# Optimization experiments

Measured on AMD Instinct MI355X. Metric: run time of the kernel, lower is better.

Reference implementation:

```python
import jax, jax.numpy as jnp
import numpy as np

D_MODEL, D_STATE, D_CONV, EXPAND = 1024, 16, 4, 2
D_INNER = EXPAND * D_MODEL  # 2048
DT_RANK = (D_MODEL + 15) // 16  # 64
BATCH, SEQ = 2, 2048


def setup_inputs() -> dict:
    key = jax.random.key(0)
    ks = jax.random.split(key, 8)
    s = 0.02
    A = jnp.tile(jnp.arange(1, D_STATE + 1, dtype=jnp.float32), (D_INNER, 1))
    return {
        "x": jax.random.normal(ks[0], (BATCH, SEQ, D_MODEL), jnp.float32),
        "in_proj_w": jax.random.normal(ks[1], (D_MODEL, 2 * D_INNER), jnp.float32) * s,
        "conv_w": jax.random.normal(ks[2], (D_INNER, 1, D_CONV), jnp.float32) * s,
        "conv_b": jnp.zeros((D_INNER,), jnp.float32),
        "x_proj_w": jax.random.normal(ks[3], (D_INNER, DT_RANK + 2 * D_STATE), jnp.float32) * s,
        "dt_proj_w": jax.random.normal(ks[4], (DT_RANK, D_INNER), jnp.float32) * s,
        "dt_proj_b": jnp.zeros((D_INNER,), jnp.float32),
        "A_log": jnp.log(A),
        "D": jnp.ones((D_INNER,), jnp.float32),
        "out_proj_w": jax.random.normal(ks[5], (D_INNER, D_MODEL), jnp.float32) * s,
    }


def _mamba(x, in_proj_w, conv_w, conv_b, x_proj_w, dt_proj_w, dt_proj_b, A_log, D, out_proj_w):
    d_inner, d_state = A_log.shape
    dt_rank = dt_proj_w.shape[0]
    seq_len = x.shape[1]

    xr = x @ in_proj_w                       # (B, L, 2*ED)
    xb, res = jnp.split(xr, 2, axis=-1)      # each (B, L, ED)

    # causal depthwise conv1d (torch pads both sides then truncates to seq_len
    # == left-pad-only causal conv)
    xc = jnp.swapaxes(xb, 1, 2)              # (B, ED, L)
    xc = jax.lax.conv_general_dilated(
        xc, conv_w, window_strides=(1,),
        padding=[(conv_w.shape[-1] - 1, 0)],
        dimension_numbers=("NCH", "OIH", "NCH"),
        feature_group_count=d_inner)
    xc = xc + conv_b[None, :, None]
    u = jax.nn.silu(jnp.swapaxes(xc, 1, 2))  # (B, L, ED)

    dbc = u @ x_proj_w                       # (B, L, dt_rank + 2*N)
    dt, Bc, Cc = jnp.split(dbc, [dt_rank, dt_rank + d_state], axis=-1)
    dt = jax.nn.softplus(dt @ dt_proj_w + dt_proj_b)  # (B, L, ED)
    A = -jnp.exp(A_log)                      # (ED, N)

    def step(h, xs):
        dt_i, B_i, C_i, u_i = xs             # (B,ED), (B,N), (B,N), (B,ED)
        dA = jnp.exp(dt_i[:, :, None] * A)   # (B, ED, N)
        h = h * dA + (dt_i * u_i)[:, :, None] * B_i[:, None, :]
        y = jnp.einsum("bdn,bn->bd", h, C_i) + D * u_i
        return h, y

    h0 = jnp.zeros((x.shape[0], d_inner, d_state), x.dtype)
    xs = (jnp.swapaxes(dt, 0, 1), jnp.swapaxes(Bc, 0, 1),
          jnp.swapaxes(Cc, 0, 1), jnp.swapaxes(u, 0, 1))
    _, ys = jax.lax.scan(step, h0, xs)       # ys: (L, B, ED)
    y_ssm = jnp.swapaxes(ys, 0, 1)           # (B, L, ED)

    y = y_ssm * jax.nn.silu(res)
    return y @ out_proj_w                    # (B, L, d_model)


def reference(x, in_proj_w, conv_w, conv_b, x_proj_w, dt_proj_w, dt_proj_b, A_log, D, out_proj_w):
    return _mamba(x, in_proj_w, conv_w, conv_b, x_proj_w, dt_proj_w, dt_proj_b, A_log, D, out_proj_w)
```

## Files before the change

### kernel.cpp

```cpp
#include <hip/hip_runtime.h>
#include <cstddef>
#include <cstdint>

#define BATCH 2
#define SEQ   2048
#define DM    1024
#define ED    2048
#define NS    16
#define DR    64
#define NROWS (BATCH*SEQ)

#define NCHUNK 64
#define CLEN   32
#define CSTATES (BATCH*ED*NS)

#define OFF_XBH   ((size_t)0)
#define OFF_RESH  ((size_t)4194304)
#define OFF_PS    ((size_t)8388608)
#define OFF_DT    ((size_t)16777216)
#define OFF_DBC   ((size_t)25165824)
#define OFF_PART  ((size_t)25559040)

typedef _Float16 half8 __attribute__((ext_vector_type(8)));
typedef _Float16 half4 __attribute__((ext_vector_type(4)));
typedef float    floatx4 __attribute__((ext_vector_type(4)));

__device__ __forceinline__ float silu_f(float x) { return x / (1.f + __expf(-x)); }

__device__ __forceinline__ void gload_lds16(const _Float16* g, _Float16* l) {
  __builtin_amdgcn_global_load_lds(
      (const __attribute__((address_space(1))) void*)g,
      (__attribute__((address_space(3))) void*)l, 16, 0, 0);
}

template<int BN, int WGM, int WGN, int EPI, int KSPLIT, int BK>
__global__ __launch_bounds__(256)
void hgemm(const _Float16* __restrict__ A, int lda,
           const _Float16* __restrict__ Bt, int ldb,
           const float* __restrict__ bias,
           float* __restrict__ C, _Float16* __restrict__ Ch,
           _Float16* __restrict__ Ch2,
           size_t cslice, int N, int K) {
  constexpr int BM = 128;
  constexpr int FM = BM / 16 / WGM;
  constexpr int FN = BN / 16 / WGN;
  constexpr int CPR = BK / 8;
  __shared__ _Float16 sA[BM * BK];
  __shared__ _Float16 sB[BN * BK];
  const int tid = threadIdx.x;
  const int ln  = tid & 63;
  const int wid = tid >> 6;
  const int wm  = wid % WGM;
  const int wn  = wid / WGM;
  const int m0  = blockIdx.y * BM;
  const int n0  = blockIdx.x * BN;
  const int l15 = ln & 15;
  const int q   = ln >> 4;

  const int kLen = K / KSPLIT;
  const int kbeg = blockIdx.z * kLen;
  if (KSPLIT > 1) C += (size_t)blockIdx.z * cslice;

  floatx4 acc[FM][FN];
  #pragma unroll
  for (int i = 0; i < FM; ++i)
    #pragma unroll
    for (int j = 0; j < FN; ++j)
      acc[i][j] = floatx4{0.f, 0.f, 0.f, 0.f};

  for (int k0 = kbeg; k0 < kbeg + kLen; k0 += BK) {
    __syncthreads();
    #pragma unroll
    for (int s = 0; s < (BM * CPR) / 256; ++s) {
      const int i = s * 256 + tid;
      const int m = i / CPR;
      const int cg = (i & (CPR - 1)) ^ ((m >> 1) & (CPR - 1));
      gload_lds16(A + (size_t)(m0 + m) * lda + k0 + cg * 8, sA + i * 8);
    }
    #pragma unroll
    for (int s = 0; s < (BN * CPR) / 256; ++s) {
      const int i = s * 256 + tid;
      const int n = i / CPR;
      const int cg = (i & (CPR - 1)) ^ ((n >> 1) & (CPR - 1));
      gload_lds16(Bt + (size_t)(n0 + n) * ldb + k0 + cg * 8, sB + i * 8);
    }
    __syncthreads();

    #pragma unroll
    for (int h = 0; h < BK / 32; ++h) {
      half8 af[FM], bf[FN];
      #pragma unroll
      for (int fm = 0; fm < FM; ++fm) {
        const int mr = wm * FM * 16 + fm * 16 + l15;
        const int cl = (h * 4 + q) ^ ((mr >> 1) & (CPR - 1));
        af[fm] = *(const half8*)(sA + mr * BK + cl * 8);
      }
      #pragma unroll
      for (int fn = 0; fn < FN; ++fn) {
        const int nr = wn * FN * 16 + fn * 16 + l15;
        const int cl = (h * 4 + q) ^ ((nr >> 1) & (CPR - 1));
        bf[fn] = *(const half8*)(sB + nr * BK + cl * 8);
      }
      #pragma unroll
      for (int fm = 0; fm < FM; ++fm)
        #pragma unroll
        for (int fn = 0; fn < FN; ++fn)
          acc[fm][fn] = __builtin_amdgcn_mfma_f32_16x16x32_f16(
              af[fm], bf[fn], acc[fm][fn], 0, 0, 0);
    }
  }

  #pragma unroll
  for (int fm = 0; fm < FM; ++fm) {
    #pragma unroll
    for (int fn = 0; fn < FN; ++fn) {
      const int col = n0 + wn * FN * 16 + fn * 16 + l15;
      #pragma unroll
      for (int r = 0; r < 4; ++r) {
        const int row = m0 + wm * FM * 16 + fm * 16 + q * 4 + r;
        float v = acc[fm][fn][r];
        if (EPI == 2) {
          if (col < ED) Ch[(size_t)row * ED + col] = (_Float16)v;
          else          Ch2[(size_t)row * ED + (col - ED)] = (_Float16)silu_f(v);
        } else if (EPI == 3) {
          v += bias[col];
          v = fmaxf(v, 0.f) + log1pf(__expf(-fabsf(v)));
          Ch[(size_t)row * N + col] = (_Float16)v;
        } else {
          C[(size_t)row * N + col] = v;
        }
      }
    }
  }
}

__device__ __forceinline__ void transpose_tile(const float* __restrict__ src,
                                               _Float16* __restrict__ dst,
                                               int R, int C, int bx, int by,
                                               int tid) {
  __shared__ float t[32][33];
  const int tx = tid & 31, ty = tid >> 5;
  const int c0 = bx * 32, r0 = by * 32;
  #pragma unroll
  for (int s = 0; s < 4; ++s)
    t[ty + s * 8][tx] = src[(size_t)(r0 + ty + s * 8) * C + c0 + tx];
  __syncthreads();
  #pragma unroll
  for (int s = 0; s < 4; ++s)
    dst[(size_t)(c0 + ty + s * 8) * R + r0 + tx] = (_Float16)t[tx][ty + s * 8];
}

#define PREP_BLOCKS 10560
__global__ __launch_bounds__(256)
void prep_kernel(const float* __restrict__ x, _Float16* __restrict__ x_h,
                 const float* __restrict__ Win, _Float16* __restrict__ Wint,
                 const float* __restrict__ Wout, _Float16* __restrict__ Woutt,
                 const float* __restrict__ Wx, _Float16* __restrict__ Wxt,
                 const float* __restrict__ Wdt, _Float16* __restrict__ Wdtt) {
  const int bid = blockIdx.x, tid = threadIdx.x;
  if (bid < 4096) {
    const int i = bid * 1024 + tid * 4;
    const float4 v = *(const float4*)(x + i);
    half4 o;
    o[0] = (_Float16)v.x; o[1] = (_Float16)v.y;
    o[2] = (_Float16)v.z; o[3] = (_Float16)v.w;
    *(half4*)(x_h + i) = o;
  } else if (bid < 8192) {
    const int t = bid - 4096;
    transpose_tile(Win, Wint, DM, 2 * ED, t & 127, t >> 7, tid);
  } else if (bid < 10240) {
    const int t = bid - 8192;
    transpose_tile(Wout, Woutt, ED, DM, t & 31, t >> 5, tid);
  } else if (bid < 10432) {
    const int t = bid - 10240;
    transpose_tile(Wx, Wxt, ED, 96, t % 3, t / 3, tid);
  } else {
    const int t = bid - 10432;
    transpose_tile(Wdt, Wdtt, DR, ED, t & 63, t >> 6, tid);
  }
}

__global__ __launch_bounds__(256)
void conv_silu_kernel(const _Float16* __restrict__ xbh, const float* __restrict__ w,
                      const float* __restrict__ cb, _Float16* __restrict__ u_h) {
  const int idx = blockIdx.x * 256 + threadIdx.x;
  const int d = idx & (ED - 1);
  const int t = (idx >> 11) & (SEQ - 1);
  const float4 wv = ((const float4*)w)[d];
  const _Float16* base = xbh + (size_t)(idx >> 11) * ED + d;
  float acc = cb[d];
  acc = fmaf(wv.w, (float)base[0], acc);
  if (t >= 1) acc = fmaf(wv.z, (float)base[-ED], acc);
  if (t >= 2) acc = fmaf(wv.y, (float)base[-2 * ED], acc);
  if (t >= 3) acc = fmaf(wv.x, (float)base[-3 * ED], acc);
  u_h[idx] = (_Float16)silu_f(acc);
}

__global__ __launch_bounds__(256)
void xproj_reduce(const float* __restrict__ part, float* __restrict__ dbc,
                  _Float16* __restrict__ dbc64h) {
  const int idx = blockIdx.x * 256 + threadIdx.x;
  float s = 0.f;
  #pragma unroll
  for (int r = 0; r < 8; ++r) s += part[(size_t)r * NROWS * 96 + idx];
  dbc[idx] = s;
  const int col = idx % 96;
  if (col < DR) dbc64h[(idx / 96) * DR + col] = (_Float16)s;
}

__device__ __forceinline__ void conv_init_h(const _Float16* xbp, int tg0,
                                            float& x1, float& x2, float& x3) {
  x1 = (tg0 >= 1) ? (float)xbp[-(int)ED] : 0.f;
  x2 = (tg0 >= 2) ? (float)xbp[-2 * (int)ED] : 0.f;
  x3 = (tg0 >= 3) ? (float)xbp[-3 * (int)ED] : 0.f;
}

__global__ __launch_bounds__(256)
void scan2_summary(const _Float16* __restrict__ dth, const _Float16* __restrict__ xbh,
                   const float* __restrict__ convw, const float* __restrict__ convb,
                   const float* __restrict__ dbc, const float* __restrict__ A_log,
                   float* __restrict__ Pbuf, float* __restrict__ Sbuf) {
  const int d = blockIdx.x * 256 + threadIdx.x;
  const int b = blockIdx.y;
  const int g = blockIdx.z;

  float Adn[16];
  {
    const float4* al = (const float4*)(A_log + (size_t)d * NS);
    #pragma unroll
    for (int i = 0; i < 4; ++i) {
      const float4 v = al[i];
      Adn[i * 4 + 0] = -__expf(v.x); Adn[i * 4 + 1] = -__expf(v.y);
      Adn[i * 4 + 2] = -__expf(v.z); Adn[i * 4 + 3] = -__expf(v.w);
    }
  }
  const float4 wv = ((const float4*)convw)[d];
  const float cbd = convb[d];

  float P[16], S[16];
  #pragma unroll
  for (int n = 0; n < 16; ++n) { P[n] = 1.f; S[n] = 0.f; }

  const int tg0 = g * CLEN;
  const size_t row0 = (size_t)b * SEQ + tg0;
  const _Float16* dtp = dth + row0 * ED + d;
  const _Float16* xbp = xbh + row0 * ED + d;
  float x1, x2, x3;
  conv_init_h(xbp, tg0, x1, x2, x3);

  for (int t = 0; t < CLEN; ++t) {
    const float xt  = (float)xbp[(size_t)t * ED];
    const float dti = (float)dtp[(size_t)t * ED];
    float cv = cbd;
    cv = fmaf(wv.w, xt, cv);
    cv = fmaf(wv.z, x1, cv);
    cv = fmaf(wv.y, x2, cv);
    cv = fmaf(wv.x, x3, cv);
    const float ui = silu_f(cv);
    x3 = x2; x2 = x1; x1 = xt;

    const float4* bc = (const float4*)(dbc + (row0 + t) * 96 + DR);
    float Bv[16];
    #pragma unroll
    for (int i = 0; i < 4; ++i) {
      const float4 v = bc[i];
      Bv[i * 4 + 0] = v.x; Bv[i * 4 + 1] = v.y;
      Bv[i * 4 + 2] = v.z; Bv[i * 4 + 3] = v.w;
    }
    const float dtu = dti * ui;
    #pragma unroll
    for (int n = 0; n < 16; ++n) {
      const float a = __expf(dti * Adn[n]);
      S[n] = fmaf(S[n], a, dtu * Bv[n]);
      P[n] *= a;
    }
  }
  const size_t c0 = (size_t)g * CSTATES + ((size_t)(b * ED + d)) * NS;
  #pragma unroll
  for (int i = 0; i < 4; ++i) {
    *(float4*)(Pbuf + c0 + i * 4) = float4{P[i*4], P[i*4+1], P[i*4+2], P[i*4+3]};
    *(float4*)(Sbuf + c0 + i * 4) = float4{S[i*4], S[i*4+1], S[i*4+2], S[i*4+3]};
  }
}

__global__ __launch_bounds__(256)
void scan2_compose(float* __restrict__ Pbuf, const float* __restrict__ Sbuf) {
  const unsigned c = blockIdx.x * 256 + threadIdx.x;
  float h = 0.f;
  for (int g = 0; g < NCHUNK; ++g) {
    const size_t idx = (size_t)g * CSTATES + c;
    const float p = Pbuf[idx], s = Sbuf[idx];
    Pbuf[idx] = h;
    h = fmaf(p, h, s);
  }
}

__global__ __launch_bounds__(256)
void scan2_apply(const _Float16* __restrict__ dth, const _Float16* __restrict__ xbh,
                 const float* __restrict__ convw, const float* __restrict__ convb,
                 const float* __restrict__ dbc, const float* __restrict__ A_log,
                 const float* __restrict__ Dp, const float* __restrict__ Pbuf,
                 _Float16* __restrict__ resh) {
  const int d = blockIdx.x * 256 + threadIdx.x;
  const int b = blockIdx.y;
  const int g = blockIdx.z;

  float Adn[16];
  {
    const float4* al = (const float4*)(A_log + (size_t)d * NS);
    #pragma unroll
    for (int i = 0; i < 4; ++i) {
      const float4 v = al[i];
      Adn[i * 4 + 0] = -__expf(v.x); Adn[i * 4 + 1] = -__expf(v.y);
      Adn[i * 4 + 2] = -__expf(v.z); Adn[i * 4 + 3] = -__expf(v.w);
    }
  }
  const float4 wv = ((const float4*)convw)[d];
  const float cbd = convb[d];
  const float Dd = Dp[d];

  float h[16];
  const size_t c0 = (size_t)g * CSTATES + ((size_t)(b * ED + d)) * NS;
  #pragma unroll
  for (int i = 0; i < 4; ++i) {
    const float4 v = *(const float4*)(Pbuf + c0 + i * 4);
    h[i * 4 + 0] = v.x; h[i * 4 + 1] = v.y;
    h[i * 4 + 2] = v.z; h[i * 4 + 3] = v.w;
  }

  const int tg0 = g * CLEN;
  const size_t row0 = (size_t)b * SEQ + tg0;
  const _Float16* dtp = dth + row0 * ED + d;
  const _Float16* xbp = xbh + row0 * ED + d;
  _Float16* rp = resh + row0 * ED + d;
  float x1, x2, x3;
  conv_init_h(xbp, tg0, x1, x2, x3);

  for (int t = 0; t < CLEN; ++t) {
    const float xt  = (float)xbp[(size_t)t * ED];
    const float dti = (float)dtp[(size_t)t * ED];
    float cv = cbd;
    cv = fmaf(wv.w, xt, cv);
    cv = fmaf(wv.z, x1, cv);
    cv = fmaf(wv.y, x2, cv);
    cv = fmaf(wv.x, x3, cv);
    const float ui = silu_f(cv);
    x3 = x2; x2 = x1; x1 = xt;

    const float4* bc = (const float4*)(dbc + (row0 + t) * 96 + DR);
    float Bv[16], Cv[16];
    #pragma unroll
    for (int i = 0; i < 4; ++i) {
      const float4 v = bc[i];
      Bv[i * 4 + 0] = v.x; Bv[i * 4 + 1] = v.y;
      Bv[i * 4 + 2] = v.z; Bv[i * 4 + 3] = v.w;
      const float4 w = bc[4 + i];
      Cv[i * 4 + 0] = w.x; Cv[i * 4 + 1] = w.y;
      Cv[i * 4 + 2] = w.z; Cv[i * 4 + 3] = w.w;
    }
    const float dtu = dti * ui;
    float y = Dd * ui;
    #pragma unroll
    for (int n = 0; n < 16; ++n) {
      const float a = __expf(dti * Adn[n]);
      h[n] = fmaf(h[n], a, dtu * Bv[n]);
      y = fmaf(h[n], Cv[n], y);
    }
    const float sres = (float)rp[(size_t)t * ED];
    rp[(size_t)t * ED] = (_Float16)(y * sres);
  }
}

extern "C" void kernel_launch(void* const* d_in, const int* in_sizes, int n_in,
                              void* d_out, int out_size, void* d_ws, size_t ws_size,
                              hipStream_t stream) {
  (void)in_sizes; (void)n_in; (void)out_size; (void)ws_size;
  const float* x     = (const float*)d_in[0];
  const float* Win   = (const float*)d_in[1];
  const float* convw = (const float*)d_in[2];
  const float* convb = (const float*)d_in[3];
  const float* Wx    = (const float*)d_in[4];
  const float* Wdt   = (const float*)d_in[5];
  const float* bdt   = (const float*)d_in[6];
  const float* Alog  = (const float*)d_in[7];
  const float* Dp    = (const float*)d_in[8];
  const float* Wout  = (const float*)d_in[9];

  float* ws   = (float*)d_ws;
  _Float16* xbh  = (_Float16*)(ws + OFF_XBH);
  _Float16* resh = (_Float16*)(ws + OFF_RESH);
  float* Pbuf = ws + OFF_PS;
  float* Sbuf = ws + OFF_PS + 4194304;
  _Float16* dth = (_Float16*)(ws + OFF_DT);
  float* dbc  = ws + OFF_DBC;
  float* part = ws + OFF_PART;
  _Float16* Woutt  = (_Float16*)(part + 3145728);
  _Float16* Wxt    = (_Float16*)(part + 4194304);
  _Float16* dbc64h = (_Float16*)(part + 4292608);
  _Float16* Wdtt   = (_Float16*)(part + 4423680);
  float* out  = (float*)d_out;

  _Float16* x_h  = (_Float16*)(ws + OFF_DT);
  _Float16* Wint = (_Float16*)(ws + OFF_DT + 2097152);
  _Float16* u_h  = (_Float16*)(ws + OFF_DT + 4194304);

  prep_kernel<<<PREP_BLOCKS, 256, 0, stream>>>(
      x, x_h, Win, Wint, Wout, Woutt, Wx, Wxt, Wdt, Wdtt);
  hgemm<128, 2, 2, 2, 1, 64><<<dim3((2 * ED) / 128, NROWS / 128), 256, 0, stream>>>(
      x_h, DM, Wint, DM, nullptr, nullptr, xbh, resh, 0, 2 * ED, DM);
  conv_silu_kernel<<<(NROWS * ED) / 256, 256, 0, stream>>>(xbh, convw, convb, u_h);
  hgemm<96, 4, 1, 0, 8, 64><<<dim3(1, NROWS / 128, 8), 256, 0, stream>>>(
      u_h, ED, Wxt, ED, nullptr, part, nullptr, nullptr, (size_t)NROWS * 96, 96, ED);
  xproj_reduce<<<(NROWS * 96) / 256, 256, 0, stream>>>(part, dbc, dbc64h);
  hgemm<128, 2, 2, 3, 1, 64><<<dim3(ED / 128, NROWS / 128), 256, 0, stream>>>(
      dbc64h, DR, Wdtt, DR, bdt, nullptr, dth, nullptr, 0, ED, DR);
  scan2_summary<<<dim3(ED / 256, BATCH, NCHUNK), 256, 0, stream>>>(
      dth, xbh, convw, convb, dbc, Alog, Pbuf, Sbuf);
  scan2_compose<<<CSTATES / 256, 256, 0, stream>>>(Pbuf, Sbuf);
  scan2_apply<<<dim3(ED / 256, BATCH, NCHUNK), 256, 0, stream>>>(
      dth, xbh, convw, convb, dbc, Alog, Dp, Pbuf, resh);
  hgemm<64, 4, 1, 0, 1, 64><<<dim3(DM / 64, NROWS / 128), 256, 0, stream>>>(
      resh, ED, Woutt, ED, nullptr, out, nullptr, nullptr, 0, DM, ED);
}
```

Before: 351.2 us.

## Fuse conv+SiLU into x_proj GEMM with atomic split-K, merge dt conversion

Removes the standalone conv_silu kernel and u_h buffer by computing the causal depthwise conv and SiLU while loading the A tile of the x_proj GEMM. The split-K partial buffer and reduce kernel are replaced by atomic adds into a dbc buffer that prep_kernel zeroes. A dedicated dt_kernel reads fp32 dbc directly, casts it to fp16 in LDS and applies bias plus softplus. Scan chunking also changes from 64x32 to 32x64, trading less summary/compose work for longer serial chunks and shrinking the workspace. The risks are redundant conv work and non-deterministic atomic summation.

```diff
diff --git a/kernel.cpp b/kernel.cpp
--- a/kernel.cpp
+++ b/kernel.cpp
@@ -10,16 +10,16 @@
 #define DR    64
 #define NROWS (BATCH*SEQ)
 
-#define NCHUNK 64
-#define CLEN   32
+#define NCHUNK 32
+#define CLEN   64
 #define CSTATES (BATCH*ED*NS)
 
 #define OFF_XBH   ((size_t)0)
 #define OFF_RESH  ((size_t)4194304)
 #define OFF_PS    ((size_t)8388608)
-#define OFF_DT    ((size_t)16777216)
-#define OFF_DBC   ((size_t)25165824)
-#define OFF_PART  ((size_t)25559040)
+#define OFF_DT    ((size_t)12582912)
+#define OFF_DBC   ((size_t)16777216)
+#define OFF_WT    ((size_t)17170432)
 
 typedef _Float16 half8 __attribute__((ext_vector_type(8)));
 typedef _Float16 half4 __attribute__((ext_vector_type(4)));
@@ -33,14 +33,12 @@
       (__attribute__((address_space(3))) void*)l, 16, 0, 0);
 }
 
-template<int BN, int WGM, int WGN, int EPI, int KSPLIT, int BK>
+template<int BN, int WGM, int WGN, int EPI, int BK>
 __global__ __launch_bounds__(256)
 void hgemm(const _Float16* __restrict__ A, int lda,
            const _Float16* __restrict__ Bt, int ldb,
-           const float* __restrict__ bias,
            float* __restrict__ C, _Float16* __restrict__ Ch,
-           _Float16* __restrict__ Ch2,
-           size_t cslice, int N, int K) {
+           _Float16* __restrict__ Ch2, int N, int K) {
   constexpr int BM = 128;
   constexpr int FM = BM / 16 / WGM;
   constexpr int FN = BN / 16 / WGN;
@@ -57,10 +55,6 @@
   const int l15 = ln & 15;
   const int q   = ln >> 4;
 
-  const int kLen = K / KSPLIT;
-  const int kbeg = blockIdx.z * kLen;
-  if (KSPLIT > 1) C += (size_t)blockIdx.z * cslice;
-
   floatx4 acc[FM][FN];
   #pragma unroll
   for (int i = 0; i < FM; ++i)
@@ -68,7 +62,7 @@
     for (int j = 0; j < FN; ++j)
       acc[i][j] = floatx4{0.f, 0.f, 0.f, 0.f};
 
-  for (int k0 = kbeg; k0 < kbeg + kLen; k0 += BK) {
+  for (int k0 = 0; k0 < K; k0 += BK) {
     __syncthreads();
     #pragma unroll
     for (int s = 0; s < (BM * CPR) / 256; ++s) {
@@ -118,17 +112,195 @@
       #pragma unroll
       for (int r = 0; r < 4; ++r) {
         const int row = m0 + wm * FM * 16 + fm * 16 + q * 4 + r;
-        float v = acc[fm][fn][r];
+        const float v = acc[fm][fn][r];
         if (EPI == 2) {
           if (col < ED) Ch[(size_t)row * ED + col] = (_Float16)v;
           else          Ch2[(size_t)row * ED + (col - ED)] = (_Float16)silu_f(v);
-        } else if (EPI == 3) {
-          v += bias[col];
-          v = fmaxf(v, 0.f) + log1pf(__expf(-fabsf(v)));
-          Ch[(size_t)row * N + col] = (_Float16)v;
         } else {
           C[(size_t)row * N + col] = v;
         }
+      }
+    }
+  }
+}
+
+__global__ __launch_bounds__(256)
+void xproj_conv_kernel(const _Float16* __restrict__ xbh,
+                       const float* __restrict__ convw,
+                       const float* __restrict__ convb,
+                       const _Float16* __restrict__ Wxt,
+                       float* __restrict__ dbc) {
+  constexpr int BM = 128, BN = 96, BK = 64, CPR = 8;
+  __shared__ _Float16 sA[BM * BK];
+  __shared__ _Float16 sB[BN * BK];
+  const int tid = threadIdx.x;
+  const int ln  = tid & 63;
+  const int wid = tid >> 6;
+  const int m0  = blockIdx.x * BM;
+  const int l15 = ln & 15;
+  const int q   = ln >> 4;
+  const int kbeg = blockIdx.y * (ED / 8);
+
+  floatx4 acc[2][6];
+  #pragma unroll
+  for (int i = 0; i < 2; ++i)
+    #pragma unroll
+    for (int j = 0; j < 6; ++j) acc[i][j] = floatx4{0.f, 0.f, 0.f, 0.f};
+
+  for (int k0 = kbeg; k0 < kbeg + ED / 8; k0 += BK) {
+    __syncthreads();
+    #pragma unroll
+    for (int s = 0; s < (BM * CPR) / 256; ++s) {
+      const int i = s * 256 + tid;
+      const int m = i / CPR;
+      const int cg = (i & (CPR - 1)) ^ ((m >> 1) & (CPR - 1));
+      const int r = m0 + m;
+      const int t = r & (SEQ - 1);
+      const int ch = k0 + cg * 8;
+      const _Float16* xp = xbh + (size_t)r * ED + ch;
+      const half8 v0 = *(const half8*)(xp);
+      half8 v1 = {}, v2 = {}, v3 = {};
+      if (t >= 1) v1 = *(const half8*)(xp - ED);
+      if (t >= 2) v2 = *(const half8*)(xp - 2 * ED);
+      if (t >= 3) v3 = *(const half8*)(xp - 3 * ED);
+      half8 o;
+      #pragma unroll
+      for (int j = 0; j < 8; ++j) {
+        const float4 wv = ((const float4*)convw)[ch + j];
+        float a = convb[ch + j];
+        a = fmaf(wv.w, (float)v0[j], a);
+        a = fmaf(wv.z, (float)v1[j], a);
+        a = fmaf(wv.y, (float)v2[j], a);
+        a = fmaf(wv.x, (float)v3[j], a);
+        o[j] = (_Float16)silu_f(a);
+      }
+      *(half8*)(sA + i * 8) = o;
+    }
+    #pragma unroll
+    for (int s = 0; s < 3; ++s) {
+      const int i = s * 256 + tid;
+      const int n = i / CPR;
+      const int cg = (i & (CPR - 1)) ^ ((n >> 1) & (CPR - 1));
+      gload_lds16(Wxt + (size_t)n * ED + k0 + cg * 8, sB + i * 8);
+    }
+    __syncthreads();
+
+    #pragma unroll
+    for (int h = 0; h < 2; ++h) {
+      half8 af[2], bf[6];
+      #pragma unroll
+      for (int fm = 0; fm < 2; ++fm) {
+        const int mr = wid * 32 + fm * 16 + l15;
+        const int cl = (h * 4 + q) ^ ((mr >> 1) & (CPR - 1));
+        af[fm] = *(const half8*)(sA + mr * BK + cl * 8);
+      }
+      #pragma unroll
+      for (int fn = 0; fn < 6; ++fn) {
+        const int nr = fn * 16 + l15;
+        const int cl = (h * 4 + q) ^ ((nr >> 1) & (CPR - 1));
+        bf[fn] = *(const half8*)(sB + nr * BK + cl * 8);
+      }
+      #pragma unroll
+      for (int fm = 0; fm < 2; ++fm)
+        #pragma unroll
+        for (int fn = 0; fn < 6; ++fn)
+          acc[fm][fn] = __builtin_amdgcn_mfma_f32_16x16x32_f16(
+              af[fm], bf[fn], acc[fm][fn], 0, 0, 0);
+    }
+  }
+
+  #pragma unroll
+  for (int fm = 0; fm < 2; ++fm) {
+    #pragma unroll
+    for (int fn = 0; fn < 6; ++fn) {
+      const int col = fn * 16 + l15;
+      #pragma unroll
+      for (int r = 0; r < 4; ++r) {
+        const int row = m0 + wid * 32 + fm * 16 + q * 4 + r;
+        unsafeAtomicAdd(&dbc[(size_t)row * 96 + col], acc[fm][fn][r]);
+      }
+    }
+  }
+}
+
+__global__ __launch_bounds__(256)
+void dt_kernel(const float* __restrict__ dbc, const _Float16* __restrict__ Wdtt,
+               const float* __restrict__ bdt, _Float16* __restrict__ dth) {
+  constexpr int BM = 128, BN = 128, BK = 64, CPR = 8;
+  __shared__ _Float16 sA[BM * BK];
+  __shared__ _Float16 sB[BN * BK];
+  const int tid = threadIdx.x;
+  const int ln  = tid & 63;
+  const int wid = tid >> 6;
+  const int wm  = wid & 1;
+  const int wn  = wid >> 1;
+  const int m0  = blockIdx.y * BM;
+  const int n0  = blockIdx.x * BN;
+  const int l15 = ln & 15;
+  const int q   = ln >> 4;
+
+  #pragma unroll
+  for (int s = 0; s < 4; ++s) {
+    const int i = s * 256 + tid;
+    const int m = i / CPR;
+    const int cg = (i & (CPR - 1)) ^ ((m >> 1) & (CPR - 1));
+    const float* p = dbc + (size_t)(m0 + m) * 96 + cg * 8;
+    const float4 a = *(const float4*)(p);
+    const float4 b = *(const float4*)(p + 4);
+    half8 o;
+    o[0] = (_Float16)a.x; o[1] = (_Float16)a.y; o[2] = (_Float16)a.z; o[3] = (_Float16)a.w;
+    o[4] = (_Float16)b.x; o[5] = (_Float16)b.y; o[6] = (_Float16)b.z; o[7] = (_Float16)b.w;
+    *(half8*)(sA + i * 8) = o;
+  }
+  #pragma unroll
+  for (int s = 0; s < 4; ++s) {
+    const int i = s * 256 + tid;
+    const int n = i / CPR;
+    const int cg = (i & (CPR - 1)) ^ ((n >> 1) & (CPR - 1));
+    gload_lds16(Wdtt + (size_t)(n0 + n) * DR + cg * 8, sB + i * 8);
+  }
+  __syncthreads();
+
+  floatx4 acc[4][4];
+  #pragma unroll
+  for (int i = 0; i < 4; ++i)
+    #pragma unroll
+    for (int j = 0; j < 4; ++j) acc[i][j] = floatx4{0.f, 0.f, 0.f, 0.f};
+
+  #pragma unroll
+  for (int h = 0; h < 2; ++h) {
+    half8 af[4], bf[4];
+    #pragma unroll
+    for (int fm = 0; fm < 4; ++fm) {
+      const int mr = wm * 64 + fm * 16 + l15;
+      const int cl = (h * 4 + q) ^ ((mr >> 1) & (CPR - 1));
+      af[fm] = *(const half8*)(sA + mr * BK + cl * 8);
+    }
+    #pragma unroll
+    for (int fn = 0; fn < 4; ++fn) {
+      const int nr = wn * 64 + fn * 16 + l15;
+      const int cl = (h * 4 + q) ^ ((nr >> 1) & (CPR - 1));
+      bf[fn] = *(const half8*)(sB + nr * BK + cl * 8);
+    }
+    #pragma unroll
+    for (int fm = 0; fm < 4; ++fm)
+      #pragma unroll
+      for (int fn = 0; fn < 4; ++fn)
+        acc[fm][fn] = __builtin_amdgcn_mfma_f32_16x16x32_f16(
+            af[fm], bf[fn], acc[fm][fn], 0, 0, 0);
+  }
+
+  #pragma unroll
+  for (int fm = 0; fm < 4; ++fm) {
+    #pragma unroll
+    for (int fn = 0; fn < 4; ++fn) {
+      const int col = n0 + wn * 64 + fn * 16 + l15;
+      #pragma unroll
+      for (int r = 0; r < 4; ++r) {
+        const int row = m0 + wm * 64 + fm * 16 + q * 4 + r;
+        float v = acc[fm][fn][r] + bdt[col];
+        v = fmaxf(v, 0.f) + log1pf(__expf(-fabsf(v)));
+        dth[(size_t)row * ED + col] = (_Float16)v;
       }
     }
   }
@@ -150,13 +322,14 @@
     dst[(size_t)(c0 + ty + s * 8) * R + r0 + tx] = (_Float16)t[tx][ty + s * 8];
 }
 
-#define PREP_BLOCKS 10560
+#define PREP_BLOCKS 10944
 __global__ __launch_bounds__(256)
 void prep_kernel(const float* __restrict__ x, _Float16* __restrict__ x_h,
                  const float* __restrict__ Win, _Float16* __restrict__ Wint,
                  const float* __restrict__ Wout, _Float16* __restrict__ Woutt,
                  const float* __restrict__ Wx, _Float16* __restrict__ Wxt,
-                 const float* __restrict__ Wdt, _Float16* __restrict__ Wdtt) {
+                 const float* __restrict__ Wdt, _Float16* __restrict__ Wdtt,
+                 float* __restrict__ dbc) {
   const int bid = blockIdx.x, tid = threadIdx.x;
   if (bid < 4096) {
     const int i = bid * 1024 + tid * 4;
@@ -174,38 +347,13 @@
   } else if (bid < 10432) {
     const int t = bid - 10240;
     transpose_tile(Wx, Wxt, ED, 96, t % 3, t / 3, tid);
-  } else {
+  } else if (bid < 10560) {
     const int t = bid - 10432;
     transpose_tile(Wdt, Wdtt, DR, ED, t & 63, t >> 6, tid);
-  }
-}
-
-__global__ __launch_bounds__(256)
-void conv_silu_kernel(const _Float16* __restrict__ xbh, const float* __restrict__ w,
-                      const float* __restrict__ cb, _Float16* __restrict__ u_h) {
-  const int idx = blockIdx.x * 256 + threadIdx.x;
-  const int d = idx & (ED - 1);
-  const int t = (idx >> 11) & (SEQ - 1);
-  const float4 wv = ((const float4*)w)[d];
-  const _Float16* base = xbh + (size_t)(idx >> 11) * ED + d;
-  float acc = cb[d];
-  acc = fmaf(wv.w, (float)base[0], acc);
-  if (t >= 1) acc = fmaf(wv.z, (float)base[-ED], acc);
-  if (t >= 2) acc = fmaf(wv.y, (float)base[-2 * ED], acc);
-  if (t >= 3) acc = fmaf(wv.x, (float)base[-3 * ED], acc);
-  u_h[idx] = (_Float16)silu_f(acc);
-}
-
-__global__ __launch_bounds__(256)
-void xproj_reduce(const float* __restrict__ part, float* __restrict__ dbc,
-                  _Float16* __restrict__ dbc64h) {
-  const int idx = blockIdx.x * 256 + threadIdx.x;
-  float s = 0.f;
-  #pragma unroll
-  for (int r = 0; r < 8; ++r) s += part[(size_t)r * NROWS * 96 + idx];
-  dbc[idx] = s;
-  const int col = idx % 96;
-  if (col < DR) dbc64h[(idx / 96) * DR + col] = (_Float16)s;
+  } else {
+    const int i = (bid - 10560) * 1024 + tid * 4;
+    *(float4*)(dbc + i) = float4{0.f, 0.f, 0.f, 0.f};
+  }
 }
 
 __device__ __forceinline__ void conv_init_h(const _Float16* xbp, int tg0,
@@ -390,35 +538,30 @@
   _Float16* xbh  = (_Float16*)(ws + OFF_XBH);
   _Float16* resh = (_Float16*)(ws + OFF_RESH);
   float* Pbuf = ws + OFF_PS;
-  float* Sbuf = ws + OFF_PS + 4194304;
+  float* Sbuf = ws + OFF_PS + 2097152;
   _Float16* dth = (_Float16*)(ws + OFF_DT);
   float* dbc  = ws + OFF_DBC;
-  float* part = ws + OFF_PART;
-  _Float16* Woutt  = (_Float16*)(part + 3145728);
-  _Float16* Wxt    = (_Float16*)(part + 4194304);
-  _Float16* dbc64h = (_Float16*)(part + 4292608);
-  _Float16* Wdtt   = (_Float16*)(part + 4423680);
+  _Float16* Woutt = (_Float16*)(ws + OFF_WT);
+  _Float16* Wxt   = (_Float16*)(ws + OFF_WT + 1048576);
+  _Float16* Wdtt  = (_Float16*)(ws + OFF_WT + 1146880);
   float* out  = (float*)d_out;
 
   _Float16* x_h  = (_Float16*)(ws + OFF_DT);
   _Float16* Wint = (_Float16*)(ws + OFF_DT + 2097152);
-  _Float16* u_h  = (_Float16*)(ws + OFF_DT + 4194304);
 
   prep_kernel<<<PREP_BLOCKS, 256, 0, stream>>>(
-      x, x_h, Win, Wint, Wout, Woutt, Wx, Wxt, Wdt, Wdtt);
-  hgemm<128, 2, 2, 2, 1, 64><<<dim3((2 * ED) / 128, NROWS / 128), 256, 0, stream>>>(
-      x_h, DM, Wint, DM, nullptr, nullptr, xbh, resh, 0, 2 * ED, DM);
-  conv_silu_kernel<<<(NROWS * ED) / 256, 256, 0, stream>>>(xbh, convw, convb, u_h);
-  hgemm<96, 4, 1, 0, 8, 64><<<dim3(1, NROWS / 128, 8), 256, 0, stream>>>(
-      u_h, ED, Wxt, ED, nullptr, part, nullptr, nullptr, (size_t)NROWS * 96, 96, ED);
-  xproj_reduce<<<(NROWS * 96) / 256, 256, 0, stream>>>(part, dbc, dbc64h);
-  hgemm<128, 2, 2, 3, 1, 64><<<dim3(ED / 128, NROWS / 128), 256, 0, stream>>>(
-      dbc64h, DR, Wdtt, DR, bdt, nullptr, dth, nullptr, 0, ED, DR);
+      x, x_h, Win, Wint, Wout, Woutt, Wx, Wxt, Wdt, Wdtt, dbc);
+  hgemm<128, 2, 2, 2, 64><<<dim3((2 * ED) / 128, NROWS / 128), 256, 0, stream>>>(
+      x_h, DM, Wint, DM, nullptr, xbh, resh, 2 * ED, DM);
+  xproj_conv_kernel<<<dim3(NROWS / 128, 8), 256, 0, stream>>>(
+      xbh, convw, convb, Wxt, dbc);
+  dt_kernel<<<dim3(ED / 128, NROWS / 128), 256, 0, stream>>>(
+      dbc, Wdtt, bdt, dth);
   scan2_summary<<<dim3(ED / 256, BATCH, NCHUNK), 256, 0, stream>>>(
       dth, xbh, convw, convb, dbc, Alog, Pbuf, Sbuf);
   scan2_compose<<<CSTATES / 256, 256, 0, stream>>>(Pbuf, Sbuf);
   scan2_apply<<<dim3(ED / 256, BATCH, NCHUNK), 256, 0, stream>>>(
       dth, xbh, convw, convb, dbc, Alog, Dp, Pbuf, resh);
-  hgemm<64, 4, 1, 0, 1, 64><<<dim3(DM / 64, NROWS / 128), 256, 0, stream>>>(
-      resh, ED, Woutt, ED, nullptr, out, nullptr, nullptr, 0, DM, ED);
-}
+  hgemm<64, 4, 1, 0, 64><<<dim3(DM / 64, NROWS / 128), 256, 0, stream>>>(
+      resh, ED, Woutt, ED, out, nullptr, nullptr, DM, ED);
+}
```

Measured after the change: 340.9 us. 2.9% less time.
